# Kernel tuning notes

Measured on AMD Instinct MI355X. Metric: run time of the kernel, lower is better.

The kernel has to match this reference:

```python
import jax, jax.numpy as jnp
import numpy as np

IN_CHANNELS = 512
NUM_HEADS = 8
PARTIAL = 4
PC = IN_CHANNELS // PARTIAL  # 128, per-branch dim


def _mha(x, wqkv, bqkv, wproj, bproj, num_heads):
    # Standard ViT-style attention block: fused qkv -> SDPA -> out proj.
    B, N, C = x.shape
    d = C // num_heads
    qkv = (x @ wqkv + bqkv).reshape(B, N, 3, num_heads, d)
    q, k, v = jnp.moveaxis(qkv, 2, 0)            # each (B, N, h, d)
    q = q.transpose(0, 2, 1, 3)                  # (B, h, N, d)
    k = k.transpose(0, 2, 1, 3)
    v = v.transpose(0, 2, 1, 3)
    scale = jnp.asarray(d, x.dtype) ** -0.5
    attn = jax.nn.softmax(jnp.einsum('bhqd,bhkd->bhqk', q, k) * scale, axis=-1)
    out = jnp.einsum('bhqk,bhkd->bhqd', attn, v)
    out = out.transpose(0, 2, 1, 3).reshape(B, N, C)
    return out @ wproj + bproj


def _channel_shuffle(x, groups):
    # ShuffleNet channel shuffle on (b, c, n, t)
    b, c, n, t = x.shape
    return x.reshape(b, groups, c // groups, n, t).transpose(0, 2, 1, 3, 4).reshape(b, c, n, t)


def setup_inputs() -> dict:
    key = jax.random.key(0)
    ks = jax.random.split(key, 13)
    b, n, t = 8, 25, 64
    inp = {'x': jax.random.normal(ks[0], (b, n, t, IN_CHANNELS), dtype=jnp.float32)}
    i = 1
    for name in ('t', 's', 'st'):
        inp[f'{name}_wqkv'] = jax.random.normal(ks[i], (PC, 3 * PC), dtype=jnp.float32) * 0.02; i += 1
        inp[f'{name}_bqkv'] = jnp.zeros((3 * PC,), dtype=jnp.float32)
        inp[f'{name}_wproj'] = jax.random.normal(ks[i], (PC, PC), dtype=jnp.float32) * 0.02; i += 1
        inp[f'{name}_bproj'] = jnp.zeros((PC,), dtype=jnp.float32)
    return inp


def reference(x, t_wqkv, t_bqkv, t_wproj, t_bproj,
              s_wqkv, s_bqkv, s_wproj, s_bproj,
              st_wqkv, st_bqkv, st_wproj, st_bproj):
    b, n, t, c = x.shape
    pc = PC
    # split order in forward: x_id, x_st, x_s, x_t (all width pc here)
    x_id = x[..., 0 * pc:1 * pc]
    x_st = x[..., 1 * pc:2 * pc]
    x_s = x[..., 2 * pc:3 * pc]
    x_t = x[..., 3 * pc:4 * pc]

    t_x = x_t.reshape(b * n, t, pc)                       # temporal: attend over t
    s_x = x_s.transpose(0, 2, 1, 3).reshape(b * t, n, pc)  # spatial: attend over n
    st_x = x_st.reshape(b, n * t, pc)                      # spatiotemporal: attend over n*t

    t_x = _mha(t_x, t_wqkv, t_bqkv, t_wproj, t_bproj, NUM_HEADS).reshape(b, n, t, pc)
    s_x = _mha(s_x, s_wqkv, s_bqkv, s_wproj, s_bproj, NUM_HEADS).reshape(b, t, n, pc).transpose(0, 2, 1, 3)
    st_x = _mha(st_x, st_wqkv, st_bqkv, st_wproj, st_bproj, NUM_HEADS).reshape(b, n, t, pc)

    # concat order: id, t, s, st (differs from split order), then to channels-first
    out = jnp.concatenate((x_id, t_x, s_x, st_x), axis=3).transpose(0, 3, 1, 2)  # (b, c, n, t)
    return _channel_shuffle(out, PARTIAL)
```

## Files before the change

kernel.cpp:

```cpp
#include <hip/hip_runtime.h>
#include <hip/hip_bf16.h>

#define BUF   1638400ull
#define QSC   0.36067376f

typedef __attribute__((ext_vector_type(4)))  float    f4;
typedef __attribute__((ext_vector_type(16))) float    f16v;
typedef __attribute__((ext_vector_type(8)))  short    s8v;
typedef __attribute__((ext_vector_type(4)))  unsigned u4v;

#if __has_builtin(__builtin_amdgcn_exp2f)
#define EXP2(x) __builtin_amdgcn_exp2f(x)
#else
#define EXP2(x) exp2f(x)
#endif
#if __has_builtin(__builtin_amdgcn_rcpf)
#define RCP(x) __builtin_amdgcn_rcpf(x)
#else
#define RCP(x) (1.0f/(x))
#endif

__device__ __forceinline__ short f2bf(float f) {
    __hip_bfloat16 h = __float2bfloat16(f);
    short s; __builtin_memcpy(&s, &h, 2); return s;
}
__device__ __forceinline__ unsigned pack2(float a, float b) {
    return (unsigned)(unsigned short)f2bf(a) | ((unsigned)(unsigned short)f2bf(b) << 16);
}
__device__ __forceinline__ float bf2f(short s) {
    return __uint_as_float((unsigned)(unsigned short)s << 16);
}
__device__ __forceinline__ unsigned tpack(float hi, float lo) {
    return __builtin_amdgcn_perm(__float_as_uint(hi), __float_as_uint(lo), 0x07060302u);
}
__device__ __forceinline__ f16v zf16() {
    f16v z;
#pragma unroll
    for (int i = 0; i < 16; i++) z[i] = 0.f;
    return z;
}

__global__ __launch_bounds__(256) void prep(
    const float* __restrict__ wq0, const float* __restrict__ wq1,
    const float* __restrict__ wq2,
    const float* __restrict__ wp0, const float* __restrict__ wp1,
    const float* __restrict__ wp2,
    short* __restrict__ wsw, short* __restrict__ onesb)
{
    const int blk = blockIdx.x, tid = threadIdx.x;
    if (blk < 96) {
        const int idx0 = blk * 2048 + tid * 8;
        const float* W; int Ncols, loc = idx0;
        if      (idx0 < 49152)  { W = wq0; Ncols = 384; }
        else if (idx0 < 98304)  { W = wq1; Ncols = 384; loc -= 49152; }
        else if (idx0 < 147456) { W = wq2; Ncols = 384; loc -= 98304; }
        else if (idx0 < 163840) { W = wp0; Ncols = 128; loc -= 147456; }
        else if (idx0 < 180224) { W = wp1; Ncols = 128; loc -= 163840; }
        else                    { W = wp2; Ncols = 128; loc -= 180224; }
        const int lane = (loc >> 3) & 63, ks = (loc >> 9) & 3, nt = loc >> 11;
        const int col = nt * 16 + (lane & 15);
        const int k0  = ks * 32 + 8 * (lane >> 4);
        s8v o;
#pragma unroll
        for (int j = 0; j < 8; j++) o[j] = f2bf(W[(k0 + j) * Ncols + col]);
        *(s8v*)(wsw + idx0) = o;
    } else {
        s8v o;
#pragma unroll
        for (int j = 0; j < 8; j++) o[j] = (short)0x3F80;
        *(s8v*)(onesb + tid * 8) = o;
    }
}

__global__ __launch_bounds__(256) void qkv_all(
    const float* __restrict__ x, const short* __restrict__ wsw,
    const float* __restrict__ bq0, const float* __restrict__ bq1,
    const float* __restrict__ bq2,
    short* __restrict__ q0, short* __restrict__ k0, short* __restrict__ vt0,
    short* __restrict__ q1, short* __restrict__ k1, short* __restrict__ vt1,
    short* __restrict__ q2, short* __restrict__ k2, short* __restrict__ vt2)
{
    const int br = blockIdx.x / 800, tile = blockIdx.x % 800;
    const int tok0 = tile * 16;
    const int wave = threadIdx.x >> 6, lane = threadIdx.x & 63;
    const int c = lane & 15, gq = lane >> 4;
    const int off = 384 - 128 * br;
    const short* wswb = wsw + br * 49152;
    const float* bias = (br == 0) ? bq0 : (br == 1) ? bq1 : bq2;

    const float* xrow = x + (size_t)(tok0 + c) * 512 + off + 8 * gq;
    s8v af[4];
#pragma unroll
    for (int ks = 0; ks < 4; ks++) {
        float4 a = *(const float4*)(xrow + ks * 32);
        float4 b = *(const float4*)(xrow + ks * 32 + 4);
        u4v t;
        t[0] = tpack(a.y, a.x); t[1] = tpack(a.w, a.z);
        t[2] = tpack(b.y, b.x); t[3] = tpack(b.w, b.z);
        af[ks] = __builtin_bit_cast(s8v, t);
    }

    const int batch0 = tok0 >> 6;
    const int b_  = tok0 / 1600;
    const int rm0 = tok0 - b_ * 1600;
    const int seq1 = rm0 >> 6;

    for (int nti = 0; nti < 6; nti++) {
        const int nt = wave * 6 + nti;
        const short* bp = wswb + ((size_t)(nt * 4) * 64 + lane) * 8;
        f4 acc = {0.f, 0.f, 0.f, 0.f};
#pragma unroll
        for (int ks = 0; ks < 4; ks++) {
            s8v bf = *(const s8v*)(bp + ks * 512);
            acc = __builtin_amdgcn_mfma_f32_16x16x32_bf16(af[ks], bf, acc, 0, 0, 0);
        }
        const float bv = bias[nt * 16 + c];
        const float v0 = acc[0]+bv, v1 = acc[1]+bv, v2 = acc[2]+bv, v3 = acc[3]+bv;
        const int which = nt >> 3, h = nt & 7;

        if (br == 0) {
            const int seq0 = (tok0 & 63) + 4 * gq;
            if (which == 2) {
                unsigned* p = (unsigned*)(vt0 + ((size_t)(batch0*8+h)*16 + c)*64 + seq0);
                p[0] = pack2(v0, v1); p[1] = pack2(v2, v3);
            } else {
                short* p = (which ? k0 : q0) + (((size_t)(batch0*8+h)*64 + seq0)*16 + c);
                p[0]=f2bf(v0); p[16]=f2bf(v1); p[32]=f2bf(v2); p[48]=f2bf(v3);
            }
        } else if (br == 1) {
            const int bt0 = b_ * 64 + (rm0 & 63) + 4 * gq;
            if (which == 2) {
                short* p = vt1 + ((size_t)(bt0*8+h)*16 + c)*32 + seq1;
                p[0]=f2bf(v0); p[4096]=f2bf(v1); p[8192]=f2bf(v2); p[12288]=f2bf(v3);
            } else {
                short* p = (which ? k1 : q1) + (((size_t)bt0*8+h)*25 + seq1)*16 + c;
                p[0]=f2bf(v0); p[3200]=f2bf(v1); p[6400]=f2bf(v2); p[9600]=f2bf(v3);
            }
        } else {
            const int seq0 = rm0 + 4 * gq;
            if (which == 2) {
                unsigned* p = (unsigned*)(vt2 + ((size_t)b_*128 + h*16 + c)*1600 + seq0);
                p[0] = pack2(v0, v1); p[1] = pack2(v2, v3);
            } else {
                short* p = (which ? k2 : q2) + (((size_t)b_*8+h)*1600 + seq0)*16 + c;
                p[0]=f2bf(v0); p[16]=f2bf(v1); p[32]=f2bf(v2); p[48]=f2bf(v3);
            }
        }
    }
}

__device__ __forceinline__ s8v load_qfrag(const short* __restrict__ qg,
                                          const int qt0, const int lane)
{
    const int n = lane & 31, g2 = lane >> 5;
    s8v qraw = *(const s8v*)(qg + (size_t)(qt0 + n) * 16 + 8 * g2);
    u4v qu;
#pragma unroll
    for (int jp = 0; jp < 4; jp++)
        qu[jp] = tpack(bf2f(qraw[2*jp+1]) * QSC, bf2f(qraw[2*jp]) * QSC);
    return __builtin_bit_cast(s8v, qu);
}

template<bool MASK>
__device__ __forceinline__ f16v attn_loop(
    const short* __restrict__ kg, const short* __restrict__ vtg, const int vstride,
    const short* __restrict__ onesb, const s8v qf, const int lane,
    const int s0, const int s1)
{
    const int n = lane & 31, g2 = lane >> 5;
    const int b4 = n >> 2;
    const int krow = ((b4 ^ (((b4 ^ (b4 >> 1)) & 1) * 3)) << 2) + (n & 3);
    const short* kp = kg + (size_t)(s0 * 32 + krow) * 16 + 8 * g2;
    const short* vp;
    int vinc;
    if (n < 16) { vp = vtg + (size_t)n * vstride + s0 * 32 + 8 * g2; vinc = 32; }
    else        { vp = onesb + 8 * g2; vinc = 0; }

    s8v kf  = *(const s8v*)kp;  kp += 512;
    s8v vf1 = *(const s8v*)vp;
    s8v vf2 = *(const s8v*)(vp + 16); vp += vinc;

    f16v oacc = zf16();
    for (int s = s0; s < s1; s++) {
        s8v kn  = *(const s8v*)kp;  kp += 512;
        s8v vn1 = *(const s8v*)vp;
        s8v vn2 = *(const s8v*)(vp + 16); vp += vinc;

        f16v sacc = __builtin_amdgcn_mfma_f32_32x32x16_bf16(kf, qf, zf16(), 0, 0, 0);

        float p[16];
#pragma unroll
        for (int r = 0; r < 16; r++) {
            p[r] = EXP2(sacc[r]);
            if (MASK && r >= 9) { if (g2) p[r] = 0.f; }
        }
        u4v u1, u2;
        u1[0]=tpack(p[1],p[0]);   u1[1]=tpack(p[3],p[2]);
        u1[2]=tpack(p[5],p[4]);   u1[3]=tpack(p[7],p[6]);
        u2[0]=tpack(p[9],p[8]);   u2[1]=tpack(p[11],p[10]);
        u2[2]=tpack(p[13],p[12]); u2[3]=tpack(p[15],p[14]);
        s8v pf1 = __builtin_bit_cast(s8v, u1);
        s8v pf2 = __builtin_bit_cast(s8v, u2);

        oacc = __builtin_amdgcn_mfma_f32_32x32x16_bf16(pf1, vf1, oacc, 0, 0, 0);
        oacc = __builtin_amdgcn_mfma_f32_32x32x16_bf16(pf2, vf2, oacc, 0, 0, 0);

        kf = kn; vf1 = vn1; vf2 = vn2;
    }
    return oacc;
}

__device__ __forceinline__ void attn_loop2(
    const short* __restrict__ kg, const short* __restrict__ vtg, const int vstride,
    const short* __restrict__ onesb, const s8v qfA, const s8v qfB, const int lane,
    const int s0, const int s1, f16v& oA, f16v& oB)
{
    const int n = lane & 31, g2 = lane >> 5;
    const int b4 = n >> 2;
    const int krow = ((b4 ^ (((b4 ^ (b4 >> 1)) & 1) * 3)) << 2) + (n & 3);
    const short* kp = kg + (size_t)(s0 * 32 + krow) * 16 + 8 * g2;
    const short* vp;
    int vinc;
    if (n < 16) { vp = vtg + (size_t)n * vstride + s0 * 32 + 8 * g2; vinc = 32; }
    else        { vp = onesb + 8 * g2; vinc = 0; }

    s8v kf  = *(const s8v*)kp;  kp += 512;
    s8v vf1 = *(const s8v*)vp;
    s8v vf2 = *(const s8v*)(vp + 16); vp += vinc;

    oA = zf16(); oB = zf16();
    for (int s = s0; s < s1; s++) {
        s8v kn  = *(const s8v*)kp;  kp += 512;
        s8v vn1 = *(const s8v*)vp;
        s8v vn2 = *(const s8v*)(vp + 16); vp += vinc;

        f16v sA = __builtin_amdgcn_mfma_f32_32x32x16_bf16(kf, qfA, zf16(), 0, 0, 0);
        f16v sB = __builtin_amdgcn_mfma_f32_32x32x16_bf16(kf, qfB, zf16(), 0, 0, 0);

        float pA[16], pB[16];
#pragma unroll
        for (int r = 0; r < 16; r++) { pA[r] = EXP2(sA[r]); pB[r] = EXP2(sB[r]); }
        u4v a1, a2, b1, b2;
        a1[0]=tpack(pA[1],pA[0]);   a1[1]=tpack(pA[3],pA[2]);
        a1[2]=tpack(pA[5],pA[4]);   a1[3]=tpack(pA[7],pA[6]);
        a2[0]=tpack(pA[9],pA[8]);   a2[1]=tpack(pA[11],pA[10]);
        a2[2]=tpack(pA[13],pA[12]); a2[3]=tpack(pA[15],pA[14]);
        b1[0]=tpack(pB[1],pB[0]);   b1[1]=tpack(pB[3],pB[2]);
        b1[2]=tpack(pB[5],pB[4]);   b1[3]=tpack(pB[7],pB[6]);
        b2[0]=tpack(pB[9],pB[8]);   b2[1]=tpack(pB[11],pB[10]);
        b2[2]=tpack(pB[13],pB[12]); b2[3]=tpack(pB[15],pB[14]);
        s8v pfA1 = __builtin_bit_cast(s8v, a1);
        s8v pfA2 = __builtin_bit_cast(s8v, a2);
        s8v pfB1 = __builtin_bit_cast(s8v, b1);
        s8v pfB2 = __builtin_bit_cast(s8v, b2);

        oA = __builtin_amdgcn_mfma_f32_32x32x16_bf16(pfA1, vf1, oA, 0, 0, 0);
        oB = __builtin_amdgcn_mfma_f32_32x32x16_bf16(pfB1, vf1, oB, 0, 0, 0);
        oA = __builtin_amdgcn_mfma_f32_32x32x16_bf16(pfA2, vf2, oA, 0, 0, 0);
        oB = __builtin_amdgcn_mfma_f32_32x32x16_bf16(pfB2, vf2, oB, 0, 0, 0);

        kf = kn; vf1 = vn1; vf2 = vn2;
    }
}

__device__ __forceinline__ void attn_epilogue(
    const f16v oacc, short* __restrict__ obase, const int orowstride,
    const int qt0, const int nq, const int lane)
{
    const int n = lane & 31, g2 = lane >> 5;
#pragma unroll
    for (int r = 0; r < 16; r++) {
        float l = __shfl_xor(oacc[r], 16);
        float o = oacc[r] * RCP(l);
        const int q = qt0 + (r & 3) + 8 * (r >> 2) + 4 * g2;
        if (n < 16 && q < nq)
            obase[(size_t)q * orowstride + n] = f2bf(o);
    }
}

__global__ __launch_bounds__(256) void attn_all(
    const short* __restrict__ q0, const short* __restrict__ k0, const short* __restrict__ vt0,
    const short* __restrict__ q1, const short* __restrict__ k1, const short* __restrict__ vt1,
    const short* __restrict__ q2, const short* __restrict__ k2, const short* __restrict__ vt2,
    const short* __restrict__ onesb,
    short* __restrict__ ob0, short* __restrict__ ob1, short* __restrict__ ob2)
{
    __shared__ float red[2][4][64][17];
    const int blk = blockIdx.x;
    const int wave = threadIdx.x >> 6, lane = threadIdx.x & 63;
    const int n = lane & 31, g2 = lane >> 5;

    if (blk < 1600) {
        const int bh = blk / 25, qt0 = (blk % 25) * 64;
        const int batch = bh >> 3, h = bh & 7;
        const short* qg = q2 + (size_t)bh * 25600;
        const s8v qfA = load_qfrag(qg, qt0, lane);
        const s8v qfB = load_qfrag(qg, qt0 + 32, lane);
        const int s0 = (50 * wave) >> 2, s1 = (50 * (wave + 1)) >> 2;
        f16v pA, pB;
        attn_loop2(k2 + (size_t)bh * 25600,
                   vt2 + (size_t)batch * 204800 + (size_t)h * 25600, 1600,
                   onesb, qfA, qfB, lane, s0, s1, pA, pB);

#pragma unroll
        for (int j = 0; j < 16; j++) {
            red[0][wave][lane][j] = pA[j];
            red[1][wave][lane][j] = pB[j];
        }
        __syncthreads();

        short* obase = ob2 + (size_t)batch * 204800 + h * 16;
#pragma unroll
        for (int qh = 0; qh < 2; qh++) {
#pragma unroll
            for (int j = 0; j < 4; j++) {
                const int r = 4 * wave + j;
                float sum = red[qh][0][lane][r] + red[qh][1][lane][r]
                          + red[qh][2][lane][r] + red[qh][3][lane][r];
                float l = __shfl_xor(sum, 16);
                float o = sum * RCP(l);
                const int q = qt0 + 32 * qh + (r & 3) + 8 * (r >> 2) + 4 * g2;
                if (n < 16)
                    obase[(size_t)q * 128 + n] = f2bf(o);
            }
        }
    } else if (blk < 2400) {
        const int wid = (blk - 1600) * 4 + wave;
        const int bh = wid >> 1, qt0 = (wid & 1) * 32;
        const int bn = bh >> 3, h = bh & 7;
        const s8v qf = load_qfrag(q0 + (size_t)bh * 1024, qt0, lane);
        f16v oacc = attn_loop<false>(k0 + (size_t)bh * 1024,
                                     vt0 + (size_t)bh * 1024, 64,
                                     onesb, qf, lane, 0, 2);
        attn_epilogue(oacc, ob0 + (size_t)bn * 8192 + h * 16, 128, qt0, 64, lane);
    } else {
        const int bh = (blk - 2400) * 4 + wave;
        const int bt = bh >> 3, h = bh & 7;
        const int b_ = bt >> 6, t_ = bt & 63;
        const s8v qf = load_qfrag(q1 + (size_t)bh * 400, 0, lane);
        f16v oacc = attn_loop<true>(k1 + (size_t)bh * 400,
                                    vt1 + (size_t)bh * 512, 32,
                                    onesb, qf, lane, 0, 1);
        attn_epilogue(oacc, ob1 + (size_t)b_ * 204800 + t_ * 128 + h * 16,
                      8192, 0, 25, lane);
    }
}

__global__ __launch_bounds__(256) void projid(
    const short* __restrict__ ob0, const short* __restrict__ ob1,
    const short* __restrict__ ob2, const short* __restrict__ wsw,
    const float* __restrict__ bp0, const float* __restrict__ bp1,
    const float* __restrict__ bp2,
    const float* __restrict__ x, float* __restrict__ out)
{
    __shared__ unsigned short xl[64 * 130];
    const int blk = blockIdx.x, tid = threadIdx.x;

    if (blk < 2400) {
        const int br = blk / 800, t8 = blk % 800;
        const short* obb = (br == 0) ? ob0 : (br == 1) ? ob1 : ob2;
        const float* bp  = (br == 0) ? bp0 : (br == 1) ? bp1 : bp2;
        const short* wswb = wsw + 147456 + br * 16384;
        const int grp = br + 1;
        const int tok0 = t8 * 16;
        const int wave = tid >> 6, lane = tid & 63;
        const int c = lane & 15, gq = lane >> 4;

        s8v af[4];
#pragma unroll
        for (int ks = 0; ks < 4; ks++)
            af[ks] = *(const s8v*)(obb + (size_t)(tok0 + c) * 128 + ks * 32 + 8 * gq);

        const int bnn = t8 >> 2, b_ = bnn / 25, n_ = bnn % 25;
        const int t0 = (t8 & 3) * 16 + 4 * gq;

        for (int nti = 0; nti < 2; nti++) {
            const int nt = wave * 2 + nti;
            const short* bpw = wswb + ((size_t)(nt * 4) * 64 + lane) * 8;
            f4 acc = {0.f, 0.f, 0.f, 0.f};
#pragma unroll
            for (int ks = 0; ks < 4; ks++) {
                s8v bf = *(const s8v*)(bpw + ks * 512);
                acc = __builtin_amdgcn_mfma_f32_16x16x32_bf16(af[ks], bf, acc, 0, 0, 0);
            }
            const int c2 = nt * 16 + c;
            const float bv = bp[c2];
            float4 st = {acc[0]+bv, acc[1]+bv, acc[2]+bv, acc[3]+bv};
            *(float4*)(out + (size_t)b_ * 819200 + (size_t)(c2 * 4 + grp) * 1600
                           + n_ * 64 + t0) = st;
        }
    } else {
        const int bn = blk - 2400;
        const int b_ = bn / 25, n_ = bn % 25;
        for (int idx = tid; idx < 8192; idx += 256) {
            int row = idx >> 7, c2 = idx & 127;
            xl[row * 130 + c2] =
                (unsigned short)(__float_as_uint(x[(size_t)(bn * 64 + row) * 512 + c2]) >> 16);
        }
        __syncthreads();
        const int t_ = tid & 63, cg = tid >> 6;
        const size_t base = (size_t)b_ * 819200 + (size_t)n_ * 64 + t_;
#pragma unroll
        for (int i = 0; i < 32; i++) {
            int c2 = cg + 4 * i;
            out[base + (size_t)(c2 * 4 + 0) * 1600] =
                __uint_as_float((unsigned)xl[t_ * 130 + c2] << 16);
        }
    }
}

extern "C" void kernel_launch(void* const* d_in, const int* in_sizes, int n_in,
                              void* d_out, int out_size, void* d_ws, size_t ws_size,
                              hipStream_t stream)
{
    const float* x        = (const float*)d_in[0];
    const float* t_wqkv   = (const float*)d_in[1];
    const float* t_bqkv   = (const float*)d_in[2];
    const float* t_wproj  = (const float*)d_in[3];
    const float* t_bproj  = (const float*)d_in[4];
    const float* s_wqkv   = (const float*)d_in[5];
    const float* s_bqkv   = (const float*)d_in[6];
    const float* s_wproj  = (const float*)d_in[7];
    const float* s_bproj  = (const float*)d_in[8];
    const float* st_wqkv  = (const float*)d_in[9];
    const float* st_bqkv  = (const float*)d_in[10];
    const float* st_wproj = (const float*)d_in[11];
    const float* st_bproj = (const float*)d_in[12];

    short* wsw   = (short*)d_ws;
    short* onesb = wsw + 196608ull;
    short* q0  = onesb + 2048ull;
    short* k0  = q0 + BUF;
    short* vt0 = k0 + BUF;
    short* q1  = vt0 + BUF;
    short* k1  = q1 + BUF;
    short* vt1 = k1 + BUF;
    short* q2  = vt1 + 2097152ull;
    short* k2  = q2 + BUF;
    short* vt2 = k2 + BUF;
    short* ob0 = vt2 + BUF;
    short* ob1 = ob0 + BUF;
    short* ob2 = ob1 + BUF;
    float* out = (float*)d_out;

    prep<<<97, 256, 0, stream>>>(t_wqkv, s_wqkv, st_wqkv,
                                 t_wproj, s_wproj, st_wproj, wsw, onesb);
    qkv_all<<<2400, 256, 0, stream>>>(x, wsw, t_bqkv, s_bqkv, st_bqkv,
                                      q0, k0, vt0, q1, k1, vt1, q2, k2, vt2);
    attn_all<<<3424, 256, 0, stream>>>(q0, k0, vt0, q1, k1, vt1, q2, k2, vt2,
                                       onesb, ob0, ob1, ob2);
    projid<<<2600, 256, 0, stream>>>(ob0, ob1, ob2, wsw,
                                     t_bproj, s_bproj, st_bproj, x, out);
}
```

Measured before the change: 171.3 us.

## Assign whole spatiotemporal query tile per wave instead of splitting keys across waves

The long spatiotemporal attention branch previously split the 50 key blocks of each 64-query tile across four waves and merged the partial sums through shared memory with a block barrier. Now each wave handles a full 64-query tile over all keys and writes output directly through the shared epilogue, and the grid shrinks accordingly. This removes the LDS reduction buffer and __syncthreads, which lowers LDS use and may raise occupancy. In exchange each wave's serial work grows fourfold and there are fewer concurrent waves for this branch (1600 waves), so latency hiding and tail balance could suffer.

```diff
diff --git a/kernel.cpp b/kernel.cpp
--- a/kernel.cpp
+++ b/kernel.cpp
@@ -285,47 +285,25 @@
     const short* __restrict__ onesb,
     short* __restrict__ ob0, short* __restrict__ ob1, short* __restrict__ ob2)
 {
-    __shared__ float red[2][4][64][17];
     const int blk = blockIdx.x;
     const int wave = threadIdx.x >> 6, lane = threadIdx.x & 63;
-    const int n = lane & 31, g2 = lane >> 5;
-
-    if (blk < 1600) {
-        const int bh = blk / 25, qt0 = (blk % 25) * 64;
+
+    if (blk < 400) {
+        const int wid = blk * 4 + wave;
+        const int bh = wid / 25, qt0 = (wid % 25) * 64;
         const int batch = bh >> 3, h = bh & 7;
         const short* qg = q2 + (size_t)bh * 25600;
         const s8v qfA = load_qfrag(qg, qt0, lane);
         const s8v qfB = load_qfrag(qg, qt0 + 32, lane);
-        const int s0 = (50 * wave) >> 2, s1 = (50 * (wave + 1)) >> 2;
-        f16v pA, pB;
+        f16v oA, oB;
         attn_loop2(k2 + (size_t)bh * 25600,
                    vt2 + (size_t)batch * 204800 + (size_t)h * 25600, 1600,
-                   onesb, qfA, qfB, lane, s0, s1, pA, pB);
-
-#pragma unroll
-        for (int j = 0; j < 16; j++) {
-            red[0][wave][lane][j] = pA[j];
-            red[1][wave][lane][j] = pB[j];
-        }
-        __syncthreads();
-
+                   onesb, qfA, qfB, lane, 0, 50, oA, oB);
         short* obase = ob2 + (size_t)batch * 204800 + h * 16;
-#pragma unroll
-        for (int qh = 0; qh < 2; qh++) {
-#pragma unroll
-            for (int j = 0; j < 4; j++) {
-                const int r = 4 * wave + j;
-                float sum = red[qh][0][lane][r] + red[qh][1][lane][r]
-                          + red[qh][2][lane][r] + red[qh][3][lane][r];
-                float l = __shfl_xor(sum, 16);
-                float o = sum * RCP(l);
-                const int q = qt0 + 32 * qh + (r & 3) + 8 * (r >> 2) + 4 * g2;
-                if (n < 16)
-                    obase[(size_t)q * 128 + n] = f2bf(o);
-            }
-        }
-    } else if (blk < 2400) {
-        const int wid = (blk - 1600) * 4 + wave;
+        attn_epilogue(oA, obase, 128, qt0,      1600, lane);
+        attn_epilogue(oB, obase, 128, qt0 + 32, 1600, lane);
+    } else if (blk < 1200) {
+        const int wid = (blk - 400) * 4 + wave;
         const int bh = wid >> 1, qt0 = (wid & 1) * 32;
         const int bn = bh >> 3, h = bh & 7;
         const s8v qf = load_qfrag(q0 + (size_t)bh * 1024, qt0, lane);
@@ -334,7 +312,7 @@
                                      onesb, qf, lane, 0, 2);
         attn_epilogue(oacc, ob0 + (size_t)bn * 8192 + h * 16, 128, qt0, 64, lane);
     } else {
-        const int bh = (blk - 2400) * 4 + wave;
+        const int bh = (blk - 1200) * 4 + wave;
         const int bt = bh >> 3, h = bh & 7;
         const int b_ = bt >> 6, t_ = bt & 63;
         const s8v qf = load_qfrag(q1 + (size_t)bh * 400, 0, lane);
@@ -447,7 +425,7 @@
                                  t_wproj, s_wproj, st_wproj, wsw, onesb);
     qkv_all<<<2400, 256, 0, stream>>>(x, wsw, t_bqkv, s_bqkv, st_bqkv,
                                       q0, k0, vt0, q1, k1, vt1, q2, k2, vt2);
-    attn_all<<<3424, 256, 0, stream>>>(q0, k0, vt0, q1, k1, vt1, q2, k2, vt2,
+    attn_all<<<2224, 256, 0, stream>>>(q0, k0, vt0, q1, k1, vt1, q2, k2, vt2,
                                        onesb, ob0, ob1, ob2);
     projid<<<2600, 256, 0, stream>>>(ob0, ob1, ob2, wsw,
                                      t_bproj, s_bproj, st_bproj, x, out);
```

After: 180.9 us. 1.06x slower.
